# Kernel tuning notes

Hardware: AMD Instinct MI355X
Metric: run time of the kernel (lower is better)

Reference implementation:

```python
import jax, jax.numpy as jnp
import numpy as np

N = 4096
IN_F = 512
OUT_F = 512


def setup_inputs() -> dict:
    key = jax.random.key(0)
    k1, k2, k3, k4 = jax.random.split(key, 4)
    x = jax.random.normal(k1, (N, IN_F), dtype=jnp.float32)
    adj = jax.random.uniform(k2, (N, N), dtype=jnp.float32)
    # linear params (torch nn.Linear default init: U(-1/sqrt(fan_in), 1/sqrt(fan_in)))
    bound = 1.0 / np.sqrt(IN_F)
    W = jax.random.uniform(k3, (OUT_F, IN_F), minval=-bound, maxval=bound, dtype=jnp.float32)
    b = jax.random.uniform(k4, (OUT_F,), minval=-bound, maxval=bound, dtype=jnp.float32)
    return {"x": x, "adj": adj, "W": W, "b": b}


def reference(x, adj, W, b):
    # adj_hat = adj + I
    adj_hat = adj + jnp.eye(adj.shape[0], dtype=adj.dtype)
    # deg is diagonal with 1/sqrt(rowsum); deg @ adj @ deg == d[:,None] * adj * d[None,:]
    d = 1.0 / jnp.sqrt(adj_hat.sum(axis=1))  # [N]
    norm_adj = d[:, None] * adj_hat * d[None, :]  # [N, N]
    h = norm_adj @ x  # [N, in_features]
    return h @ W.T + b  # [N, out_features]
```

## Files before the change

kernel.cpp:

```cpp
#include <hip/hip_runtime.h>
#include <cstdint>

#define NN 4096
#define FF 512

typedef short bf16x8 __attribute__((ext_vector_type(8)));
typedef float f32x16 __attribute__((ext_vector_type(16)));

__device__ __forceinline__ uint16_t f2bf(float f) {
    uint32_t u = __builtin_bit_cast(uint32_t, f);
    u += 0x7FFFu + ((u >> 16) & 1u);
    return (uint16_t)(u >> 16);
}

__global__ __launch_bounds__(256) void k_prep(const float* __restrict__ adj,
                                              float* __restrict__ d,
                                              uint16_t* __restrict__ Abf) {
    const int row  = blockIdx.x * 4 + (threadIdx.x >> 6);
    const int lane = threadIdx.x & 63;
    const float4* p = (const float4*)(adj + (size_t)row * NN);
    float4 v[16];
    float s = 0.f;
#pragma unroll
    for (int i = 0; i < 16; ++i) {
        v[i] = p[lane + i * 64];
        s += (v[i].x + v[i].y) + (v[i].z + v[i].w);
    }
#pragma unroll
    for (int off = 1; off < 64; off <<= 1) s += __shfl_xor(s, off);
    const float di = rsqrtf(s + 1.0f);
    if (lane == 0) d[row] = di;
    uint16_t* outp = Abf + (size_t)row * NN;
#pragma unroll
    for (int i = 0; i < 16; ++i) {
        const int cb = (lane + i * 64) * 4;
        float a0 = v[i].x, a1 = v[i].y, a2 = v[i].z, a3 = v[i].w;
        if (cb + 0 == row) a0 += 1.0f;
        if (cb + 1 == row) a1 += 1.0f;
        if (cb + 2 == row) a2 += 1.0f;
        if (cb + 3 == row) a3 += 1.0f;
        ushort4 o;
        o.x = f2bf(a0); o.y = f2bf(a1); o.z = f2bf(a2); o.w = f2bf(a3);
        *(ushort4*)(outp + cb) = o;
    }
}

__global__ __launch_bounds__(256) void k_xc(const float* __restrict__ x,
                                            uint16_t* __restrict__ xbf) {
    const size_t t4 = (size_t)blockIdx.x * 256 + threadIdx.x;
    float4 v = *(const float4*)(x + t4 * 4);
    ushort4 o;
    o.x = f2bf(v.x); o.y = f2bf(v.y); o.z = f2bf(v.z); o.w = f2bf(v.w);
    *(ushort4*)(xbf + t4 * 4) = o;
}

__global__ __launch_bounds__(256) void k_wc(const float* __restrict__ W,
                                            uint16_t* __restrict__ Wbf) {
    const size_t t4 = (size_t)blockIdx.x * 256 + threadIdx.x;
    float4 v = *(const float4*)(W + t4 * 4);
    ushort4 o;
    o.x = f2bf(v.x); o.y = f2bf(v.y); o.z = f2bf(v.z); o.w = f2bf(v.w);
    *(ushort4*)(Wbf + t4 * 4) = o;
}

__global__ __launch_bounds__(256) void k_zt(const float* __restrict__ z32,
                                            const float* __restrict__ d,
                                            uint16_t* __restrict__ zdT) {
    __shared__ uint16_t t[64][72];
    const int k0 = blockIdx.x * 64;
    const int n0 = blockIdx.y * 64;
    const int tid = threadIdx.x;
    const int r   = tid >> 4;
    const int c4  = tid & 15;
#pragma unroll
    for (int pass = 0; pass < 4; ++pass) {
        const int row = pass * 16 + r;
        float4 v = *(const float4*)(z32 + (size_t)(k0 + row) * FF + n0 + c4 * 4);
        const float dk = d[k0 + row];
        t[c4 * 4 + 0][row] = f2bf(v.x * dk);
        t[c4 * 4 + 1][row] = f2bf(v.y * dk);
        t[c4 * 4 + 2][row] = f2bf(v.z * dk);
        t[c4 * 4 + 3][row] = f2bf(v.w * dk);
    }
    __syncthreads();
#pragma unroll
    for (int pass = 0; pass < 2; ++pass) {
        const int cid = pass * 256 + tid;
        const int n  = cid >> 3;
        const int ch = cid & 7;
        *(uint4*)(zdT + (size_t)(n0 + n) * NN + k0 + ch * 8) = *(const uint4*)&t[n][ch * 8];
    }
}

template <int BM, int BN, int K, int SPLITK>
__global__ __launch_bounds__(512, 2) void k_mm(const uint16_t* __restrict__ A,
                                               const uint16_t* __restrict__ Bt,
                                               float* __restrict__ outp) {
    constexpr int MT    = NN / BM;
    constexpr int NTC   = FF / BN;
    constexpr int KSLEN = K / SPLITK;
    constexpr int NT    = KSLEN / 64;
    constexpr int MTX   = MT / 8;
    constexpr int MF    = BM / 128;
    constexpr int NF    = BN / 64;
    constexpr int LPT_A = BM / 64;
    constexpr int LPT_B = BN / 64;
    constexpr int LPT   = LPT_A + LPT_B;

    __shared__ uint16_t As[2][BM * 64];
    __shared__ uint16_t Bs[2][BN * 64];

    const int id   = blockIdx.x;
    const int slot = id >> 3;
    const int mt   = (id & 7) * MTX + slot / (NTC * SPLITK);
    const int rem  = slot % (NTC * SPLITK);
    const int nt   = rem % NTC;
    const int ks   = rem / NTC;
    const int m0 = mt * BM;
    const int n0 = nt * BN;
    const int k0 = ks * KSLEN;

    const int tid  = threadIdx.x;
    const int w    = tid >> 6;
    const int lane = tid & 63;
    const int wm = w >> 1, wn = w & 1;

    f32x16 acc[MF][NF] = {};

    auto STAGE = [&](int t, int buf) {
        const int ktb = k0 + t * 64;
#pragma unroll
        for (int i = 0; i < LPT_A; ++i) {
            const int boff = i * 8192 + tid * 16;
            const int row  = boff >> 7;
            const int q    = (boff >> 4) & 7;
            const int c    = q ^ (row & 7);
            const uint16_t* src = A + (size_t)(m0 + row) * K + ktb + c * 8;
            __builtin_amdgcn_global_load_lds(
                (const __attribute__((address_space(1))) void*)src,
                (__attribute__((address_space(3))) void*)&As[buf][boff >> 1],
                16, 0, 0);
        }
#pragma unroll
        for (int i = 0; i < LPT_B; ++i) {
            const int boff = i * 8192 + tid * 16;
            const int row  = boff >> 7;
            const int q    = (boff >> 4) & 7;
            const int c    = q ^ (row & 7);
            const uint16_t* src = Bt + (size_t)(n0 + row) * K + ktb + c * 8;
            __builtin_amdgcn_global_load_lds(
                (const __attribute__((address_space(1))) void*)src,
                (__attribute__((address_space(3))) void*)&Bs[buf][boff >> 1],
                16, 0, 0);
        }
    };

    auto COMPUTE = [&](int buf) {
#pragma unroll
        for (int ksl = 0; ksl < 4; ++ksl) {
            const int cl = ksl * 2 + (lane >> 5);
            bf16x8 af[MF], bfr[NF];
#pragma unroll
            for (int mf = 0; mf < MF; ++mf) {
                const int r = wm * (MF * 32) + mf * 32 + (lane & 31);
                af[mf] = *(const bf16x8*)&As[buf][r * 64 + ((cl ^ (r & 7)) << 3)];
            }
#pragma unroll
            for (int nf = 0; nf < NF; ++nf) {
                const int r = wn * (NF * 32) + nf * 32 + (lane & 31);
                bfr[nf] = *(const bf16x8*)&Bs[buf][r * 64 + ((cl ^ (r & 7)) << 3)];
            }
#pragma unroll
            for (int mf = 0; mf < MF; ++mf)
#pragma unroll
                for (int nf = 0; nf < NF; ++nf)
                    acc[mf][nf] = __builtin_amdgcn_mfma_f32_32x32x16_bf16(
                        af[mf], bfr[nf], acc[mf][nf], 0, 0, 0);
        }
    };

    STAGE(0, 0);
    for (int t = 0; t < NT - 1; ++t) {
        STAGE(t + 1, (t + 1) & 1);
        if constexpr (LPT == 6) asm volatile("s_waitcnt vmcnt(6)" ::: "memory");
        else                    asm volatile("s_waitcnt vmcnt(3)" ::: "memory");
        __builtin_amdgcn_s_barrier();
        COMPUTE(t & 1);
        __builtin_amdgcn_s_barrier();
    }
    asm volatile("s_waitcnt vmcnt(0)" ::: "memory");
    __builtin_amdgcn_s_barrier();
    COMPUTE((NT - 1) & 1);

    float* dst = outp + (size_t)ks * NN * FF;
    const int rb = m0 + wm * (MF * 32) + ((lane >> 5) << 2);
    const int cb = n0 + wn * (NF * 32) + (lane & 31);
#pragma unroll
    for (int mf = 0; mf < MF; ++mf) {
#pragma unroll
        for (int nf = 0; nf < NF; ++nf) {
            const int gcol = cb + nf * 32;
#pragma unroll
            for (int r = 0; r < 16; ++r) {
                const int grow = rb + mf * 32 + (r & 3) + ((r >> 2) << 3);
                dst[(size_t)grow * FF + gcol] = acc[mf][nf][r];
            }
        }
    }
}

__global__ __launch_bounds__(256) void k_red(const float* __restrict__ parts,
                                             const float* __restrict__ d,
                                             const float* __restrict__ b,
                                             float* __restrict__ out) {
    constexpr size_t STRIDE = (size_t)NN * FF;
    const size_t g   = (size_t)blockIdx.x * 256 + threadIdx.x;
    const int    row = (int)((g * 4) >> 9);
    const int    col = (int)((g * 4) & 511);
    float4 s = *(const float4*)(parts + g * 4);
#pragma unroll
    for (int p = 1; p < 4; ++p) {
        float4 v = *(const float4*)(parts + p * STRIDE + g * 4);
        s.x += v.x; s.y += v.y; s.z += v.z; s.w += v.w;
    }
    const float di = d[row];
    const float4 bv = *(const float4*)(b + col);
    float4 o;
    o.x = s.x * di + bv.x;
    o.y = s.y * di + bv.y;
    o.z = s.z * di + bv.z;
    o.w = s.w * di + bv.w;
    *(float4*)(out + g * 4) = o;
}

extern "C" void kernel_launch(void* const* d_in, const int* in_sizes, int n_in,
                              void* d_out, int out_size, void* d_ws, size_t ws_size,
                              hipStream_t stream) {
    const float* x   = (const float*)d_in[0];
    const float* adj = (const float*)d_in[1];
    const float* W   = (const float*)d_in[2];
    const float* b   = (const float*)d_in[3];
    float* out = (float*)d_out;

    char* ws = (char*)d_ws;
    float*    d_    = (float*)ws;
    uint16_t* Abf   = (uint16_t*)(ws + 65536);
    uint16_t* zdT   = Abf + (size_t)NN * NN;
    uint16_t* xbf   = zdT + (size_t)FF * NN;
    uint16_t* Wbf   = xbf + (size_t)NN * FF;
    float*    z32   = (float*)(Wbf + (size_t)FF * FF);
    float*    parts = z32 + (size_t)NN * FF;

    k_wc<<<FF * FF / 1024, 256, 0, stream>>>(W, Wbf);
    k_xc<<<NN * FF / 1024, 256, 0, stream>>>(x, xbf);
    k_prep<<<NN / 4, 256, 0, stream>>>(adj, d_, Abf);
    k_mm<128, 64, FF, 1><<<256, 512, 0, stream>>>(xbf, Wbf, z32);
    k_zt<<<dim3(NN / 64, FF / 64), 256, 0, stream>>>(z32, d_, zdT);
    k_mm<256, 128, NN, 4><<<256, 512, 0, stream>>>(Abf, zdT, parts);
    k_red<<<NN * FF / 1024, 256, 0, stream>>>(parts, d_, b, out);
}
```

Measured before the change: 71.19 us.

## Shrink GEMM tiles to 128-row, 32-wide K steps with 16x16x32 MFMA, single buffer

Replaces the double-buffered 256x128 / 64-wide-K GEMM tiles with 128-row tiles, 32-wide K steps, a single LDS buffer, 256-thread blocks and 16x16x32 bf16 MFMA instructions, and doubles the grid size. The aim appears to be simpler code, higher occupancy and more blocks. In exchange it drops the load/compute overlap of the double buffer, adds two __syncthreads per K step, and lowers data reuse per tile, so global and LDS traffic per FLOP rises.

```diff
diff --git a/kernel.cpp b/kernel.cpp
--- a/kernel.cpp
+++ b/kernel.cpp
@@ -5,7 +5,7 @@
 #define FF 512
 
 typedef short bf16x8 __attribute__((ext_vector_type(8)));
-typedef float f32x16 __attribute__((ext_vector_type(16)));
+typedef float f32x4 __attribute__((ext_vector_type(4)));
 
 __device__ __forceinline__ uint16_t f2bf(float f) {
     uint32_t u = __builtin_bit_cast(uint32_t, f);
@@ -92,23 +92,21 @@
     }
 }
 
-template <int BM, int BN, int K, int SPLITK>
-__global__ __launch_bounds__(512, 2) void k_mm(const uint16_t* __restrict__ A,
-                                               const uint16_t* __restrict__ Bt,
-                                               float* __restrict__ outp) {
+template <int BN, int K, int SPLITK>
+__global__ __launch_bounds__(256) void k_mm(const uint16_t* __restrict__ A,
+                                            const uint16_t* __restrict__ Bt,
+                                            float* __restrict__ outp) {
+    constexpr int BM    = 128;
     constexpr int MT    = NN / BM;
     constexpr int NTC   = FF / BN;
     constexpr int KSLEN = K / SPLITK;
-    constexpr int NT    = KSLEN / 64;
+    constexpr int NT    = KSLEN / 32;
     constexpr int MTX   = MT / 8;
-    constexpr int MF    = BM / 128;
-    constexpr int NF    = BN / 64;
-    constexpr int LPT_A = BM / 64;
+    constexpr int NF    = BN / 32;
     constexpr int LPT_B = BN / 64;
-    constexpr int LPT   = LPT_A + LPT_B;
-
-    __shared__ uint16_t As[2][BM * 64];
-    __shared__ uint16_t Bs[2][BN * 64];
+
+    __shared__ uint16_t As[BM * 32];
+    __shared__ uint16_t Bs[BN * 32];
 
     const int id   = blockIdx.x;
     const int slot = id >> 3;
@@ -125,85 +123,71 @@
     const int lane = tid & 63;
     const int wm = w >> 1, wn = w & 1;
 
-    f32x16 acc[MF][NF] = {};
-
-    auto STAGE = [&](int t, int buf) {
-        const int ktb = k0 + t * 64;
-#pragma unroll
-        for (int i = 0; i < LPT_A; ++i) {
-            const int boff = i * 8192 + tid * 16;
-            const int row  = boff >> 7;
-            const int q    = (boff >> 4) & 7;
-            const int c    = q ^ (row & 7);
+    f32x4 acc[4][NF] = {};
+
+    for (int t = 0; t < NT; ++t) {
+        const int ktb = k0 + t * 32;
+#pragma unroll
+        for (int i = 0; i < 2; ++i) {
+            const int boff = i * 4096 + tid * 16;
+            const int row  = boff >> 6;
+            const int q    = (boff >> 4) & 3;
+            const int c    = q ^ (row & 3);
             const uint16_t* src = A + (size_t)(m0 + row) * K + ktb + c * 8;
             __builtin_amdgcn_global_load_lds(
                 (const __attribute__((address_space(1))) void*)src,
-                (__attribute__((address_space(3))) void*)&As[buf][boff >> 1],
+                (__attribute__((address_space(3))) void*)&As[boff >> 1],
                 16, 0, 0);
         }
 #pragma unroll
         for (int i = 0; i < LPT_B; ++i) {
-            const int boff = i * 8192 + tid * 16;
-            const int row  = boff >> 7;
-            const int q    = (boff >> 4) & 7;
-            const int c    = q ^ (row & 7);
+            const int boff = i * 4096 + tid * 16;
+            const int row  = boff >> 6;
+            const int q    = (boff >> 4) & 3;
+            const int c    = q ^ (row & 3);
             const uint16_t* src = Bt + (size_t)(n0 + row) * K + ktb + c * 8;
             __builtin_amdgcn_global_load_lds(
                 (const __attribute__((address_space(1))) void*)src,
-                (__attribute__((address_space(3))) void*)&Bs[buf][boff >> 1],
+                (__attribute__((address_space(3))) void*)&Bs[boff >> 1],
                 16, 0, 0);
         }
-    };
-
-    auto COMPUTE = [&](int buf) {
-#pragma unroll
-        for (int ksl = 0; ksl < 4; ++ksl) {
-            const int cl = ksl * 2 + (lane >> 5);
-            bf16x8 af[MF], bfr[NF];
-#pragma unroll
-            for (int mf = 0; mf < MF; ++mf) {
-                const int r = wm * (MF * 32) + mf * 32 + (lane & 31);
-                af[mf] = *(const bf16x8*)&As[buf][r * 64 + ((cl ^ (r & 7)) << 3)];
+        __syncthreads();
+
+        {
+            const int cl = lane >> 4;
+            bf16x8 af[4], bfr[NF];
+#pragma unroll
+            for (int mf = 0; mf < 4; ++mf) {
+                const int r = wm * 64 + mf * 16 + (lane & 15);
+                af[mf] = *(const bf16x8*)&As[r * 32 + ((cl ^ (r & 3)) << 3)];
             }
 #pragma unroll
             for (int nf = 0; nf < NF; ++nf) {
-                const int r = wn * (NF * 32) + nf * 32 + (lane & 31);
-                bfr[nf] = *(const bf16x8*)&Bs[buf][r * 64 + ((cl ^ (r & 7)) << 3)];
+                const int r = wn * (NF * 16) + nf * 16 + (lane & 15);
+                bfr[nf] = *(const bf16x8*)&Bs[r * 32 + ((cl ^ (r & 3)) << 3)];
             }
 #pragma unroll
-            for (int mf = 0; mf < MF; ++mf)
+            for (int mf = 0; mf < 4; ++mf)
 #pragma unroll
                 for (int nf = 0; nf < NF; ++nf)
-                    acc[mf][nf] = __builtin_amdgcn_mfma_f32_32x32x16_bf16(
+                    acc[mf][nf] = __builtin_amdgcn_mfma_f32_16x16x32_bf16(
                         af[mf], bfr[nf], acc[mf][nf], 0, 0, 0);
         }
-    };
-
-    STAGE(0, 0);
-    for (int t = 0; t < NT - 1; ++t) {
-        STAGE(t + 1, (t + 1) & 1);
-        if constexpr (LPT == 6) asm volatile("s_waitcnt vmcnt(6)" ::: "memory");
-        else                    asm volatile("s_waitcnt vmcnt(3)" ::: "memory");
-        __builtin_amdgcn_s_barrier();
-        COMPUTE(t & 1);
-        __builtin_amdgcn_s_barrier();
-    }
-    asm volatile("s_waitcnt vmcnt(0)" ::: "memory");
-    __builtin_amdgcn_s_barrier();
-    COMPUTE((NT - 1) & 1);
+        __syncthreads();
+    }
 
     float* dst = outp + (size_t)ks * NN * FF;
-    const int rb = m0 + wm * (MF * 32) + ((lane >> 5) << 2);
-    const int cb = n0 + wn * (NF * 32) + (lane & 31);
-#pragma unroll
-    for (int mf = 0; mf < MF; ++mf) {
+    const int rbase = m0 + wm * 64 + ((lane >> 4) << 2);
+    const int cbase = n0 + wn * (NF * 16) + (lane & 15);
+#pragma unroll
+    for (int mf = 0; mf < 4; ++mf) {
 #pragma unroll
         for (int nf = 0; nf < NF; ++nf) {
-            const int gcol = cb + nf * 32;
-#pragma unroll
-            for (int r = 0; r < 16; ++r) {
-                const int grow = rb + mf * 32 + (r & 3) + ((r >> 2) << 3);
-                dst[(size_t)grow * FF + gcol] = acc[mf][nf][r];
+            const int col = cbase + nf * 16;
+#pragma unroll
+            for (int r = 0; r < 4; ++r) {
+                const int row = rbase + mf * 16 + r;
+                dst[(size_t)row * FF + col] = acc[mf][nf][r];
             }
         }
     }
@@ -254,8 +238,8 @@
     k_wc<<<FF * FF / 1024, 256, 0, stream>>>(W, Wbf);
     k_xc<<<NN * FF / 1024, 256, 0, stream>>>(x, xbf);
     k_prep<<<NN / 4, 256, 0, stream>>>(adj, d_, Abf);
-    k_mm<128, 64, FF, 1><<<256, 512, 0, stream>>>(xbf, Wbf, z32);
+    k_mm<64, FF, 1><<<512, 256, 0, stream>>>(xbf, Wbf, z32);
     k_zt<<<dim3(NN / 64, FF / 64), 256, 0, stream>>>(z32, d_, zdT);
-    k_mm<256, 128, NN, 4><<<256, 512, 0, stream>>>(Abf, zdT, parts);
+    k_mm<128, NN, 4><<<512, 256, 0, stream>>>(Abf, zdT, parts);
     k_red<<<NN * FF / 1024, 256, 0, stream>>>(parts, d_, b, out);
 }
```

New measurement: 80.69 us. +13.3%, slower.
